# Performance work log

Measured on AMD Instinct MI355X. Metric: run time of the kernel, lower is better.

Reference implementation:

```python
import jax, jax.numpy as jnp
import numpy as np

EMBED = 1024
HEADS = 16
HEAD_DIM = EMBED // HEADS
LN_EPS = 1e-5
XNORM_GAMMA = 0.01


def xnorm(x, gamma):
    # x * gamma / ||x||_4 along last dim (keepdim)
    norm4 = jnp.sum(x ** 4, axis=-1, keepdims=True) ** 0.25
    return x * gamma / norm4


def setup_inputs() -> dict:
    key = jax.random.key(0)
    ks = jax.random.split(key, 12)
    B, S = 2, 2048
    sc_hd = 1.0 / np.sqrt(HEAD_DIM)
    sc_e = 1.0 / np.sqrt(EMBED)
    return {
        "value": jax.random.normal(ks[0], (B, S, EMBED), jnp.float32),
        "key": jax.random.normal(ks[1], (B, S, EMBED), jnp.float32),
        "query": jax.random.normal(ks[2], (B, S, EMBED), jnp.float32),
        # per-head projections, torch Linear convention: y = x @ W.T
        "Wq": jax.random.normal(ks[3], (HEAD_DIM, HEAD_DIM), jnp.float32) * sc_hd,
        "Wk": jax.random.normal(ks[4], (HEAD_DIM, HEAD_DIM), jnp.float32) * sc_hd,
        "Wv": jax.random.normal(ks[5], (HEAD_DIM, HEAD_DIM), jnp.float32) * sc_hd,
        "Wo": jax.random.normal(ks[6], (EMBED, EMBED), jnp.float32) * sc_e,
        "bo": jnp.zeros((EMBED,), jnp.float32),
        "ln_w": jnp.ones((EMBED,), jnp.float32),
        "ln_b": jnp.zeros((EMBED,), jnp.float32),
        "Wsq": jax.random.normal(ks[7], (EMBED, EMBED), jnp.float32) * sc_e,
        "bsq": jnp.zeros((EMBED,), jnp.float32),
    }


def reference(value, key, query, Wq, Wk, Wv, Wo, bo, ln_w, ln_b, Wsq, bsq):
    B, S, E = query.shape
    # split heads: [B, S, H, D]
    v = value.reshape(B, S, HEADS, HEAD_DIM)
    k = key.reshape(B, S, HEADS, HEAD_DIM)
    q = query.reshape(B, S, HEADS, HEAD_DIM)
    v = jnp.einsum('nshd,ed->nshe', v, Wv)
    k = jnp.einsum('nshd,ed->nshe', k, Wk)
    q = jnp.einsum('nshd,ed->nshe', q, Wq)
    # energy: [B, H, Sq, Sk]
    energy = jnp.einsum('nqhd,nkhd->nhqk', q, k)
    energy_n = xnorm(energy, XNORM_GAMMA)
    v_n = xnorm(v, XNORM_GAMMA)
    out = jnp.einsum('nhql,nlhd->nqhd', energy_n, v_n).reshape(B, S, E)
    attn = out @ Wo.T + bo
    # LayerNorm(attention + query) over embed dim
    x = attn + query
    mu = jnp.mean(x, axis=-1, keepdims=True)
    var = jnp.mean((x - mu) ** 2, axis=-1, keepdims=True)
    x = (x - mu) / jnp.sqrt(var + LN_EPS) * ln_w + ln_b
    # SE gating: x * sigmoid(Linear(x))
    gate = jax.nn.sigmoid(x @ Wsq.T + bsq)
    return x * gate
```

## Files before the change

kernel.cpp:

```cpp
#include <hip/hip_runtime.h>
#include <stdint.h>

#define B_ 2
#define S_ 2048
#define E_ 1024
#define H_ 16
#define HD_ 64
#define N_ (B_*S_)
#define BH_ (B_*H_)
#define GAMMA 0.01f

typedef __attribute__((ext_vector_type(8))) short bf16x8;
typedef __attribute__((ext_vector_type(4))) float f32x4;
typedef __attribute__((ext_vector_type(2))) float f32x2;
typedef __attribute__((ext_vector_type(16))) float f32x16;
typedef __attribute__((ext_vector_type(4))) unsigned int u32x4;
typedef unsigned short u16;
typedef unsigned int u32;

#define SWZ(row, kb) ((kb) ^ (((row)&7)<<4))

__device__ __forceinline__ u16 f2bf(float f){
  union { float f; u32 u; } v; v.f = f;
  return (u16)((v.u + 0x7FFFu + ((v.u>>16)&1u)) >> 16);
}

__device__ __forceinline__ float bf2f(u16 u){
  union { u32 u; float f; } v; v.u = ((u32)u)<<16; return v.f;
}

__device__ __forceinline__ u32 cvt_pk_bf16(float lo, float hi){
  u32 r; asm("v_cvt_pk_bf16_f32 %0, %1, %2" : "=v"(r) : "v"(lo), "v"(hi)); return r;
}

__device__ __forceinline__ uint4 pack8(float4 a, float4 b){
  uint4 r;
  r.x = (u32)f2bf(a.x) | ((u32)f2bf(a.y)<<16);
  r.y = (u32)f2bf(a.z) | ((u32)f2bf(a.w)<<16);
  r.z = (u32)f2bf(b.x) | ((u32)f2bf(b.y)<<16);
  r.w = (u32)f2bf(b.z) | ((u32)f2bf(b.w)<<16);
  return r;
}

__device__ __forceinline__ bf16x8 ldfrag(const unsigned char* base, int row, int kbyte){
  return *reinterpret_cast<const bf16x8*>(base + row*128 + SWZ(row, kbyte));
}

__device__ __forceinline__ void gl_lds16(const void* g, void* l){
  __builtin_amdgcn_global_load_lds(
      (const __attribute__((address_space(1))) unsigned int*)g,
      (__attribute__((address_space(3))) unsigned int*)l, 16, 0, 0);
}

__global__ __launch_bounds__(256) void k_cvt(const float* __restrict__ Wo, const float* __restrict__ Wsq,
                                             u16* __restrict__ wo16, u16* __restrict__ wsq16)
{
  int gid = blockIdx.x*256 + threadIdx.x;
  int n4 = (E_*E_)/4;
  const float4* src; ushort4* dst; int i;
  if (gid < n4){ src = (const float4*)Wo;  dst = (ushort4*)wo16;  i = gid; }
  else         { src = (const float4*)Wsq; dst = (ushort4*)wsq16; i = gid - n4; }
  float4 v = src[i];
  ushort4 p; p.x = f2bf(v.x); p.y = f2bf(v.y); p.z = f2bf(v.z); p.w = f2bf(v.w);
  dst[i] = p;
}

__device__ __forceinline__ void proj_mfma(const unsigned char* X, const unsigned char* W,
                                          int wid, int l15, int g4, f32x4 acc[4])
{
  f32x4 z = {0.f,0.f,0.f,0.f};
  acc[0]=z; acc[1]=z; acc[2]=z; acc[3]=z;
  #pragma unroll
  for (int kk=0;kk<2;++kk){
    int kbyte = kk*64 + g4*16;
    bf16x8 a = ldfrag(X, wid*16 + l15, kbyte);
    #pragma unroll
    for (int t=0;t<4;++t){
      bf16x8 w = ldfrag(W, t*16 + l15, kbyte);
      acc[t] = __builtin_amdgcn_mfma_f32_16x16x32_bf16(a, w, acc[t], 0, 0, 0);
    }
  }
}

__global__ __launch_bounds__(256) void k_proj(
    const float* __restrict__ qin, const float* __restrict__ kin, const float* __restrict__ vin,
    const float* __restrict__ Wq, const float* __restrict__ Wk, const float* __restrict__ Wv,
    u16* __restrict__ qp, u16* __restrict__ kp, u16* __restrict__ vnT)
{
  __shared__ alignas(16) unsigned char sm[57344];
  const int XQ=0, XK=8192, XV=16384, WQS=24576, WKS=32768, WVS=40960, VT=49152;
  int tid = threadIdx.x, lane = tid&63, wid = tid>>6;
  int l15 = lane&15, g4 = lane>>4;
  int tb = blockIdx.x*64;
  int h  = blockIdx.y;
  int b  = tb >> 11;
  int sbase = tb & 2047;
  int bh = b*H_ + h;

  {
    int rl = tid>>2;
    int d0 = (tid&3)*16;
    const float* xs[3] = { qin, kin, vin };
    const float* wsrc[3] = { Wq, Wk, Wv };
    const int xoff[3] = {XQ,XK,XV}, woff[3] = {WQS,WKS,WVS};
    #pragma unroll
    for (int m3=0;m3<3;++m3){
      const float4* gx = reinterpret_cast<const float4*>(xs[m3] + (size_t)(tb+rl)*E_ + h*HD_ + d0);
      float4 a=gx[0], bb=gx[1], c=gx[2], d=gx[3];
      *(uint4*)(sm + xoff[m3] + rl*128 + SWZ(rl, d0*2))    = pack8(a,bb);
      *(uint4*)(sm + xoff[m3] + rl*128 + SWZ(rl, d0*2+16)) = pack8(c,d);
      const float4* gw = reinterpret_cast<const float4*>(wsrc[m3] + rl*64 + d0);
      float4 e=gw[0], f=gw[1], g2=gw[2], h2=gw[3];
      *(uint4*)(sm + woff[m3] + rl*128 + SWZ(rl, d0*2))    = pack8(e,f);
      *(uint4*)(sm + woff[m3] + rl*128 + SWZ(rl, d0*2+16)) = pack8(g2,h2);
    }
  }
  __syncthreads();

  f32x4 acc[4];
  proj_mfma(sm+XQ, sm+WQS, wid, l15, g4, acc);
  #pragma unroll
  for (int t=0;t<4;++t)
    #pragma unroll
    for (int r=0;r<4;++r){
      int tokl = wid*16 + g4*4 + r;
      qp[((size_t)bh*S_ + sbase + tokl)*HD_ + t*16 + l15] = f2bf(acc[t][r]);
    }
  proj_mfma(sm+XK, sm+WKS, wid, l15, g4, acc);
  #pragma unroll
  for (int t=0;t<4;++t)
    #pragma unroll
    for (int r=0;r<4;++r){
      int tokl = wid*16 + g4*4 + r;
      kp[((size_t)bh*S_ + sbase + tokl)*HD_ + t*16 + l15] = f2bf(acc[t][r]);
    }
  proj_mfma(sm+XV, sm+WVS, wid, l15, g4, acc);
  {
    float p4r[4] = {0.f,0.f,0.f,0.f};
    #pragma unroll
    for (int t=0;t<4;++t)
      #pragma unroll
      for (int r=0;r<4;++r){ float e = acc[t][r]; float e2 = e*e; p4r[r] += e2*e2; }
    #pragma unroll
    for (int r=0;r<4;++r){
      float p = p4r[r];
      p += __shfl_xor(p,1); p += __shfl_xor(p,2); p += __shfl_xor(p,4); p += __shfl_xor(p,8);
      p4r[r] = GAMMA / sqrtf(sqrtf(p));
    }
    #pragma unroll
    for (int t=0;t<4;++t)
      #pragma unroll
      for (int r=0;r<4;++r){
        int tokl = wid*16 + g4*4 + r;
        int dd = t*16 + l15;
        *(u16*)(sm + VT + dd*128 + SWZ(dd, tokl*2)) = f2bf(acc[t][r] * p4r[r]);
      }
  }
  __syncthreads();
  {
    int dd = tid>>2; int c2 = tid&3;
    size_t gbase = ((size_t)bh*HD_ + dd)*S_ + sbase + c2*16;
    uint4 v0 = *(const uint4*)(sm + VT + dd*128 + SWZ(dd, c2*32));
    uint4 v1 = *(const uint4*)(sm + VT + dd*128 + SWZ(dd, c2*32+16));
    *(uint4*)(vnT + gbase)     = v0;
    *(uint4*)(vnT + gbase + 8) = v1;
  }
}

__global__ __launch_bounds__(256, 2) void k_attn(
    const u16* __restrict__ qp, const u16* __restrict__ kp,
    const u16* __restrict__ vnT, u16* __restrict__ ao)
{
  __shared__ alignas(128) unsigned char sm[49152];
  char* smc = (char*)sm;
  int tid = threadIdx.x, lane = tid&63, wv = tid>>6;
  int l31 = lane&31, hi = lane>>5;
  int qi = wv>>1, kj = wv&1;
  int L = blockIdx.x;
  int xcd = L&7, iw = L>>3;
  int bh = xcd*4 + (iw&3);
  int qx = iw>>2;
  int qb = qx*128;
  int b = bh>>4, h = bh&15;
  const u16* Kb = kp  + (size_t)bh*S_*HD_;
  const u16* Vb = vnT + (size_t)bh*HD_*S_;
  const u16* Qb = qp  + (size_t)bh*S_*HD_;
  int q0 = qb + qi*64;

  bf16x8 qf[2][4];
  #pragma unroll
  for (int f=0;f<2;++f)
    #pragma unroll
    for (int kk=0;kk<4;++kk)
      qf[f][kk] = *reinterpret_cast<const bf16x8*>(Qb + (size_t)(q0 + f*32 + l31)*HD_ + kk*16 + hi*8);

  f32x16 z16 = {};
  f32x16 o[2][2];
  #pragma unroll
  for (int f=0;f<2;++f){ o[f][0] = z16; o[f][1] = z16; }
  f32x2 p4a[2] = {{0.f,0.f},{0.f,0.f}};

  int off0 = wv*2048 + lane*16;
  int row0 = off0 >> 7, col0 = (off0 & 127) ^ ((row0 & 7) << 4);
  int off1 = off0 + 1024;
  int row1 = off1 >> 7, col1 = (off1 & 127) ^ ((row1 & 7) << 4);
  const char* kSrc0 = (const char*)Kb + row0*128 + col0;
  const char* kSrc1 = (const char*)Kb + row1*128 + col1;
  const char* vSrc0 = (const char*)Vb + (size_t)row0*4096 + col0;
  const char* vSrc1 = (const char*)Vb + (size_t)row1*4096 + col1;
  unsigned dOfs = wv*2048;

  auto STAGE = [&](int bsel, int kt){
    char* db = smc + bsel*16384 + dOfs;
    gl_lds16(kSrc0 + (size_t)kt*8192, db);
    gl_lds16(kSrc1 + (size_t)kt*8192, db + 1024);
    gl_lds16(vSrc0 + (size_t)kt*128,  db + 8192);
    gl_lds16(vSrc1 + (size_t)kt*128,  db + 8192 + 1024);
  };

  auto PACK = [&](const f32x16& e, u32 (&w)[4][2], f32x2& pa){
    #pragma unroll
    for (int j=0;j<8;++j){
      const int g=j>>1, i=j&1;
      float a = e[4*g+2*i], c = e[4*g+2*i+1];
      f32x2 pr = {a, c};
      f32x2 e2;
      asm("v_pk_mul_f32 %0, %1, %1" : "=v"(e2) : "v"(pr));
      asm("v_pk_fma_f32 %0, %1, %1, %0" : "+v"(pa) : "v"(e2));
      w[g][i] = cvt_pk_bf16(a, c);
    }
  };
  auto AFRAG = [&](u32 (&w)[4][2], int s) -> bf16x8 {
    u32 a0 = w[2*s][0], b0 = w[2*s+1][0];
    u32 a1 = w[2*s][1], b1 = w[2*s+1][1];
    asm("v_permlane32_swap_b32 %0, %1" : "+v"(a0), "+v"(b0));
    asm("v_permlane32_swap_b32 %0, %1" : "+v"(a1), "+v"(b1));
    u32x4 fw = {a0, a1, b0, b1};
    return __builtin_bit_cast(bf16x8, fw);
  };

  auto QK = [&](const unsigned char* K_, f32x16& E0, f32x16& E1){
    bf16x8 ka[4];
    #pragma unroll
    for (int kk=0;kk<4;++kk) ka[kk] = ldfrag(K_, kj*32 + l31, kk*32 + hi*16);
    E0 = z16; E1 = z16;
    __builtin_amdgcn_s_setprio(1);
    #pragma unroll
    for (int kk=0;kk<4;++kk){
      E0 = __builtin_amdgcn_mfma_f32_32x32x16_bf16(ka[kk], qf[0][kk], E0, 0,0,0);
      E1 = __builtin_amdgcn_mfma_f32_32x32x16_bf16(ka[kk], qf[1][kk], E1, 0,0,0);
    }
    __builtin_amdgcn_s_setprio(0);
  };

  auto PVF = [&](const unsigned char* V_, u32 (&w0)[4][2], u32 (&w1)[4][2]){
    bf16x8 vb[2][2];
    #pragma unroll
    for (int s=0;s<2;++s){
      vb[s][0] = ldfrag(V_, l31,    kj*64 + s*32 + hi*16);
      vb[s][1] = ldfrag(V_, 32+l31, kj*64 + s*32 + hi*16);
    }
    __builtin_amdgcn_s_setprio(1);
    #pragma unroll
    for (int s=0;s<2;++s){
      bf16x8 ef0 = AFRAG(w0, s);
      bf16x8 ef1 = AFRAG(w1, s);
      o[0][0] = __builtin_amdgcn_mfma_f32_32x32x16_bf16(ef0, vb[s][0], o[0][0], 0,0,0);
      o[0][1] = __builtin_amdgcn_mfma_f32_32x32x16_bf16(ef0, vb[s][1], o[0][1], 0,0,0);
      o[1][0] = __builtin_amdgcn_mfma_f32_32x32x16_bf16(ef1, vb[s][0], o[1][0], 0,0,0);
      o[1][1] = __builtin_amdgcn_mfma_f32_32x32x16_bf16(ef1, vb[s][1], o[1][1], 0,0,0);
    }
    __builtin_amdgcn_s_setprio(0);
  };

  const int NT = S_/64;
  STAGE(0, 0); STAGE(1, 1);
  asm volatile("s_waitcnt vmcnt(4)" ::: "memory");
  __builtin_amdgcn_s_barrier();
  asm volatile("" ::: "memory");
  STAGE(2, 2);

  f32x16 eA0, eA1, eB0, eB1;
  u32 w0[4][2], w1[4][2];
  QK(sm + 0*16384, eA0, eA1);

  #pragma unroll 1
  for (int t=0; t<NT; t+=2){
    const unsigned char* B0 = sm + (t%3)*16384;
    const unsigned char* B1 = sm + ((t+1)%3)*16384;
    PACK(eA0, w0, p4a[0]);
    PACK(eA1, w1, p4a[1]);
    PVF(B0 + 8192, w0, w1);
    if (t+1 < NT-1) { asm volatile("s_waitcnt vmcnt(4)" ::: "memory"); }
    else            { asm volatile("s_waitcnt vmcnt(0)" ::: "memory"); }
    __builtin_amdgcn_s_barrier();
    asm volatile("" ::: "memory");
    QK(B1, eB0, eB1);
    if (t+3 < NT) STAGE((t+3)%3, t+3);
    PACK(eB0, w0, p4a[0]);
    PACK(eB1, w1, p4a[1]);
    PVF(B1 + 8192, w0, w1);
    if (t+2 < NT){
      if (t+2 < NT-1) { asm volatile("s_waitcnt vmcnt(4)" ::: "memory"); }
      else            { asm volatile("s_waitcnt vmcnt(0)" ::: "memory"); }
      __builtin_amdgcn_s_barrier();
      asm volatile("" ::: "memory");
      QK(sm + ((t+2)%3)*16384, eA0, eA1);
      if (t+4 < NT) STAGE((t+4)%3, t+4);
    }
  }

  float p4f[2];
  #pragma unroll
  for (int f=0;f<2;++f) p4f[f] = p4a[f].x + p4a[f].y;

  __syncthreads();
  float* red  = (float*)smc;
  float* redp = (float*)(smc + 32768);
  if (kj==1){
    #pragma unroll
    for (int f=0;f<2;++f){
      #pragma unroll
      for (int ds=0;ds<2;++ds){
        float* dst = red + ((((qi*2+f)*2+ds)*64 + lane)*16);
        #pragma unroll
        for (int r4=0;r4<4;++r4)
          *(float4*)(dst + r4*4) = make_float4(o[f][ds][r4*4],o[f][ds][r4*4+1],o[f][ds][r4*4+2],o[f][ds][r4*4+3]);
      }
      redp[(qi*2+f)*64 + lane] = p4f[f];
    }
  }
  __syncthreads();
  if (kj==0){
    #pragma unroll
    for (int f=0;f<2;++f){
      #pragma unroll
      for (int ds=0;ds<2;++ds){
        const float* srcp = red + ((((qi*2+f)*2+ds)*64 + lane)*16);
        #pragma unroll
        for (int r4=0;r4<4;++r4){
          float4 t = *(const float4*)(srcp + r4*4);
          o[f][ds][r4*4]+=t.x; o[f][ds][r4*4+1]+=t.y; o[f][ds][r4*4+2]+=t.z; o[f][ds][r4*4+3]+=t.w;
        }
      }
      p4f[f] += redp[(qi*2+f)*64 + lane];
      p4f[f] += __shfl_xor(p4f[f], 32);
    }
    float sc0 = GAMMA * rsqrtf(sqrtf(p4f[0]));
    float sc1 = GAMMA * rsqrtf(sqrtf(p4f[1]));
    #pragma unroll
    for (int f=0;f<2;++f){
      #pragma unroll
      for (int r=0;r<16;++r){
        int qrow = (r&3) + 8*(r>>2) + 4*hi;
        float scr = __shfl(f==0 ? sc0 : sc1, qrow);
        size_t n = (size_t)b*S_ + q0 + f*32 + qrow;
        u16* dst = ao + n*E_ + h*HD_;
        dst[l31]    = f2bf(o[f][0][r] * scr);
        dst[32+l31] = f2bf(o[f][1][r] * scr);
      }
    }
  }
}

template<int MODE>
__global__ __launch_bounds__(256, 2) void k_gemm(
    const u16* __restrict__ A, const u16* __restrict__ Bw,
    const float* __restrict__ bias, const float* __restrict__ auxf,
    const u16* __restrict__ aux16, float* __restrict__ out32, u16* __restrict__ out16)
{
  __shared__ alignas(128) unsigned char sm[73728];
  char* smc = (char*)sm;
  int tid = threadIdx.x, lane = tid&63, wv = tid>>6;
  int l31 = lane&31, hi = lane>>5;
  int wr = wv>>1, wc = wv&1;
  int LL = (blockIdx.x & 7)*64 + (blockIdx.x >> 3);
  int mt = LL >> 4, nt = LL & 15;
  int m0 = mt*128, n0 = nt*64;

  int ric  = lane>>3;
  int colb = ((lane&7)*16) ^ ((ric&7)<<4);
  const char* aSrc[4]; const char* bSrc[2];
  #pragma unroll
  for (int j=0;j<4;++j)
    aSrc[j] = (const char*)A  + ((size_t)(m0 + wv*32 + 8*j + ric)*E_)*2 + colb;
  #pragma unroll
  for (int j=0;j<2;++j)
    bSrc[j] = (const char*)Bw + ((size_t)(n0 + wv*16 + 8*j + ric)*E_)*2 + colb;

  auto STAGE = [&](int bsel, int t){
    char* db = smc + bsel*24576;
    size_t kb2 = (size_t)t*128;
    #pragma unroll
    for (int j=0;j<4;++j) gl_lds16(aSrc[j] + kb2, db + (wv*4+j)*1024);
    #pragma unroll
    for (int j=0;j<2;++j) gl_lds16(bSrc[j] + kb2, db + 16384 + (wv*2+j)*1024);
  };

  f32x16 acc[2] = {{}, {}};

  const int NK = E_/64;
  STAGE(0, 0); STAGE(1, 1);

  #pragma unroll 1
  for (int t=0; t<NK; ++t){
    if (t < NK-1) { asm volatile("s_waitcnt vmcnt(6)" ::: "memory"); }
    else          { asm volatile("s_waitcnt vmcnt(0)" ::: "memory"); }
    __builtin_amdgcn_s_barrier();
    asm volatile("" ::: "memory");
    if (t+2 < NK) STAGE((t+2)%3, t+2);

    const unsigned char* Ap_ = sm + (t%3)*24576;
    const unsigned char* Bp_ = Ap_ + 16384;
    #pragma unroll
    for (int kk=0;kk<4;++kk){
      bf16x8 bfr = ldfrag(Bp_, wc*32 + l31, kk*32 + hi*16);
      bf16x8 af0 = ldfrag(Ap_, wr*64 + l31,      kk*32 + hi*16);
      bf16x8 af1 = ldfrag(Ap_, wr*64 + 32 + l31, kk*32 + hi*16);
      __builtin_amdgcn_s_setprio(1);
      acc[0] = __builtin_amdgcn_mfma_f32_32x32x16_bf16(af0, bfr, acc[0], 0,0,0);
      acc[1] = __builtin_amdgcn_mfma_f32_32x32x16_bf16(af1, bfr, acc[1], 0,0,0);
      __builtin_amdgcn_s_setprio(0);
    }
  }

  int col = n0 + wc*32 + l31;
  float bi = bias[col];
  #pragma unroll
  for (int rg=0;rg<2;++rg)
    #pragma unroll
    for (int r=0;r<16;++r){
      int mrow = m0 + wr*64 + rg*32 + (r&3) + 8*(r>>2) + 4*hi;
      size_t idx = (size_t)mrow*E_ + col;
      float v = acc[rg][r] + bi;
      if (MODE == 0){
        out16[idx] = f2bf(v + auxf[idx]);
      } else {
        float gg = 1.f/(1.f + __expf(-v));
        out32[idx] = bf2f(aux16[idx]) * gg;
      }
    }
}

__global__ __launch_bounds__(256) void k_ln(
    const u16* __restrict__ xin, const float* __restrict__ lnw, const float* __restrict__ lnb,
    u16* __restrict__ xout)
{
  __shared__ float red[8];
  __shared__ float stats[2];
  int row = blockIdx.x, tid = threadIdx.x;
  ushort4 xr = reinterpret_cast<const ushort4*>(xin + (size_t)row*E_)[tid];
  float x0 = bf2f(xr.x), x1 = bf2f(xr.y), x2 = bf2f(xr.z), x3 = bf2f(xr.w);
  float s  = x0 + x1 + x2 + x3;
  float s2 = x0*x0 + x1*x1 + x2*x2 + x3*x3;
  #pragma unroll
  for (int m=1;m<64;m<<=1){ s += __shfl_xor(s,m); s2 += __shfl_xor(s2,m); }
  if ((tid&63)==0){ red[tid>>6] = s; red[4+(tid>>6)] = s2; }
  __syncthreads();
  if (tid==0){
    float ts  = red[0]+red[1]+red[2]+red[3];
    float ts2 = red[4]+red[5]+red[6]+red[7];
    float mu  = ts * (1.f/E_);
    float var = ts2 * (1.f/E_) - mu*mu;
    stats[0] = mu; stats[1] = rsqrtf(var + 1e-5f);
  }
  __syncthreads();
  float mu = stats[0], rstd = stats[1];
  float4 w  = reinterpret_cast<const float4*>(lnw)[tid];
  float4 bb = reinterpret_cast<const float4*>(lnb)[tid];
  ushort4 p;
  p.x = f2bf((x0-mu)*rstd*w.x + bb.x);
  p.y = f2bf((x1-mu)*rstd*w.y + bb.y);
  p.z = f2bf((x2-mu)*rstd*w.z + bb.z);
  p.w = f2bf((x3-mu)*rstd*w.w + bb.w);
  reinterpret_cast<ushort4*>(xout + (size_t)row*E_)[tid] = p;
}

extern "C" void kernel_launch(void* const* d_in, const int* in_sizes, int n_in,
                              void* d_out, int out_size, void* d_ws, size_t ws_size,
                              hipStream_t stream)
{
  const float* value = (const float*)d_in[0];
  const float* key   = (const float*)d_in[1];
  const float* query = (const float*)d_in[2];
  const float* Wq    = (const float*)d_in[3];
  const float* Wk    = (const float*)d_in[4];
  const float* Wv    = (const float*)d_in[5];
  const float* Wo    = (const float*)d_in[6];
  const float* bo    = (const float*)d_in[7];
  const float* lnw   = (const float*)d_in[8];
  const float* lnb   = (const float*)d_in[9];
  const float* Wsq   = (const float*)d_in[10];
  const float* bsq   = (const float*)d_in[11];
  float* out = (float*)d_out;

  char* ws = (char*)d_ws;
  const size_t MB = 1ull<<20;
  u16*   qp     = (u16*)(ws + 0*MB);
  u16*   kp     = (u16*)(ws + 8*MB);
  u16*   vnT    = (u16*)(ws + 16*MB);
  u16*   ao     = (u16*)(ws + 24*MB);
  u16*   xres16 = (u16*)(ws + 8*MB);
  u16*   x16    = (u16*)(ws + 16*MB);
  u16*   wo16   = (u16*)(ws + 48*MB);
  u16*   wsq16  = (u16*)(ws + 50*MB);

  k_cvt <<<2048, 256, 0, stream>>>(Wo, Wsq, wo16, wsq16);
  k_proj<<<dim3(N_/64, H_), 256, 0, stream>>>(query, key, value, Wq, Wk, Wv, qp, kp, vnT);
  k_attn<<<512, 256, 0, stream>>>(qp, kp, vnT, ao);
  k_gemm<0><<<512, 256, 0, stream>>>(ao, wo16, bo, query, (const u16*)nullptr, (float*)nullptr, xres16);
  k_ln  <<<N_, 256, 0, stream>>>(xres16, lnw, lnb, x16);
  k_gemm<1><<<512, 256, 0, stream>>>(x16, wsq16, bsq, (const float*)nullptr, x16, out, (u16*)nullptr);
}
```

Before: 109.5 us.

## Fuse weight conversion into projection kernel and double-buffer 128-key attention tiles

The standalone bf16 weight-conversion kernel is folded into k_proj as 128 extra blocks, which removes one launch. The attention kernel now stages 128-key K/V tiles in a two-buffer ring (64KB LDS) instead of 64-key tiles in a three-buffer ring. It does two QK/PV sub-steps per barrier, with a new 256-byte-row swizzle for V and separate p4 accumulators. The block-to-(bh,q) mapping changes so consecutive blocks on an XCD share a head. The goal is fewer barriers and less launch overhead, at the cost of more LDS, which may limit the two-blocks-per-CU occupancy, and less prefetch depth.

```diff
diff --git a/kernel.cpp b/kernel.cpp
--- a/kernel.cpp
+++ b/kernel.cpp
@@ -45,24 +45,14 @@
 __device__ __forceinline__ bf16x8 ldfrag(const unsigned char* base, int row, int kbyte){
   return *reinterpret_cast<const bf16x8*>(base + row*128 + SWZ(row, kbyte));
 }
+__device__ __forceinline__ bf16x8 ldfragV(const unsigned char* base, int row, int col){
+  return *reinterpret_cast<const bf16x8*>(base + row*256 + (col ^ ((row&15)<<4)));
+}
 
 __device__ __forceinline__ void gl_lds16(const void* g, void* l){
   __builtin_amdgcn_global_load_lds(
       (const __attribute__((address_space(1))) unsigned int*)g,
       (__attribute__((address_space(3))) unsigned int*)l, 16, 0, 0);
-}
-
-__global__ __launch_bounds__(256) void k_cvt(const float* __restrict__ Wo, const float* __restrict__ Wsq,
-                                             u16* __restrict__ wo16, u16* __restrict__ wsq16)
-{
-  int gid = blockIdx.x*256 + threadIdx.x;
-  int n4 = (E_*E_)/4;
-  const float4* src; ushort4* dst; int i;
-  if (gid < n4){ src = (const float4*)Wo;  dst = (ushort4*)wo16;  i = gid; }
-  else         { src = (const float4*)Wsq; dst = (ushort4*)wsq16; i = gid - n4; }
-  float4 v = src[i];
-  ushort4 p; p.x = f2bf(v.x); p.y = f2bf(v.y); p.z = f2bf(v.z); p.w = f2bf(v.w);
-  dst[i] = p;
 }
 
 __device__ __forceinline__ void proj_mfma(const unsigned char* X, const unsigned char* W,
@@ -85,9 +75,24 @@
 __global__ __launch_bounds__(256) void k_proj(
     const float* __restrict__ qin, const float* __restrict__ kin, const float* __restrict__ vin,
     const float* __restrict__ Wq, const float* __restrict__ Wk, const float* __restrict__ Wv,
-    u16* __restrict__ qp, u16* __restrict__ kp, u16* __restrict__ vnT)
+    u16* __restrict__ qp, u16* __restrict__ kp, u16* __restrict__ vnT,
+    const float* __restrict__ Wo, const float* __restrict__ Wsq,
+    u16* __restrict__ wo16, u16* __restrict__ wsq16)
 {
   __shared__ alignas(16) unsigned char sm[57344];
+  if (blockIdx.y >= H_){
+    int cblk = (blockIdx.y - H_)*64 + blockIdx.x;
+    int n4 = (E_*E_)/4;
+    for (int i = cblk*256 + threadIdx.x; i < 2*n4; i += 128*256){
+      const float4* src; ushort4* dst; int j;
+      if (i < n4){ src=(const float4*)Wo;  dst=(ushort4*)wo16;  j=i; }
+      else       { src=(const float4*)Wsq; dst=(ushort4*)wsq16; j=i-n4; }
+      float4 v = src[j];
+      ushort4 p; p.x=f2bf(v.x); p.y=f2bf(v.y); p.z=f2bf(v.z); p.w=f2bf(v.w);
+      dst[j] = p;
+    }
+    return;
+  }
   const int XQ=0, XK=8192, XV=16384, WQS=24576, WKS=32768, WVS=40960, VT=49152;
   int tid = threadIdx.x, lane = tid&63, wid = tid>>6;
   int l15 = lane&15, g4 = lane>>4;
@@ -171,15 +176,15 @@
     const u16* __restrict__ qp, const u16* __restrict__ kp,
     const u16* __restrict__ vnT, u16* __restrict__ ao)
 {
-  __shared__ alignas(128) unsigned char sm[49152];
+  __shared__ alignas(128) unsigned char sm[65536];
   char* smc = (char*)sm;
   int tid = threadIdx.x, lane = tid&63, wv = tid>>6;
   int l31 = lane&31, hi = lane>>5;
   int qi = wv>>1, kj = wv&1;
   int L = blockIdx.x;
   int xcd = L&7, iw = L>>3;
-  int bh = xcd*4 + (iw&3);
-  int qx = iw>>2;
+  int bh = xcd*4 + (iw>>4);
+  int qx = iw&15;
   int qb = qx*128;
   int b = bh>>4, h = bh&15;
   const u16* Kb = kp  + (size_t)bh*S_*HD_;
@@ -199,23 +204,25 @@
   #pragma unroll
   for (int f=0;f<2;++f){ o[f][0] = z16; o[f][1] = z16; }
   f32x2 p4a[2] = {{0.f,0.f},{0.f,0.f}};
-
-  int off0 = wv*2048 + lane*16;
-  int row0 = off0 >> 7, col0 = (off0 & 127) ^ ((row0 & 7) << 4);
-  int off1 = off0 + 1024;
-  int row1 = off1 >> 7, col1 = (off1 & 127) ^ ((row1 & 7) << 4);
-  const char* kSrc0 = (const char*)Kb + row0*128 + col0;
-  const char* kSrc1 = (const char*)Kb + row1*128 + col1;
-  const char* vSrc0 = (const char*)Vb + (size_t)row0*4096 + col0;
-  const char* vSrc1 = (const char*)Vb + (size_t)row1*4096 + col1;
-  unsigned dOfs = wv*2048;
+  f32x2 p4b[2] = {{0.f,0.f},{0.f,0.f}};
+
+  const char* kSrcC[4]; const char* vSrcC[4];
+  #pragma unroll
+  for (int c=0;c<4;++c){
+    int rk = wv*32 + c*8 + (lane>>3);
+    int ck = ((lane&7)*16) ^ ((rk&7)<<4);
+    kSrcC[c] = (const char*)Kb + (size_t)rk*128 + ck;
+    int rv = wv*16 + c*4 + (lane>>4);
+    int cv = ((lane&15)*16) ^ ((rv&15)<<4);
+    vSrcC[c] = (const char*)Vb + (size_t)rv*4096 + cv;
+  }
 
   auto STAGE = [&](int bsel, int kt){
-    char* db = smc + bsel*16384 + dOfs;
-    gl_lds16(kSrc0 + (size_t)kt*8192, db);
-    gl_lds16(kSrc1 + (size_t)kt*8192, db + 1024);
-    gl_lds16(vSrc0 + (size_t)kt*128,  db + 8192);
-    gl_lds16(vSrc1 + (size_t)kt*128,  db + 8192 + 1024);
+    char* db = smc + bsel*32768 + wv*4096;
+    #pragma unroll
+    for (int c=0;c<4;++c) gl_lds16(kSrcC[c] + (size_t)kt*16384, db + c*1024);
+    #pragma unroll
+    for (int c=0;c<4;++c) gl_lds16(vSrcC[c] + (size_t)kt*256,   db + 16384 + c*1024);
   };
 
   auto PACK = [&](const f32x16& e, u32 (&w)[4][2], f32x2& pa){
@@ -239,10 +246,10 @@
     return __builtin_bit_cast(bf16x8, fw);
   };
 
-  auto QK = [&](const unsigned char* K_, f32x16& E0, f32x16& E1){
+  auto QK = [&](const unsigned char* K_, int s2, f32x16& E0, f32x16& E1){
     bf16x8 ka[4];
     #pragma unroll
-    for (int kk=0;kk<4;++kk) ka[kk] = ldfrag(K_, kj*32 + l31, kk*32 + hi*16);
+    for (int kk=0;kk<4;++kk) ka[kk] = ldfrag(K_, kj*64 + s2*32 + l31, kk*32 + hi*16);
     E0 = z16; E1 = z16;
     __builtin_amdgcn_s_setprio(1);
     #pragma unroll
@@ -253,12 +260,12 @@
     __builtin_amdgcn_s_setprio(0);
   };
 
-  auto PVF = [&](const unsigned char* V_, u32 (&w0)[4][2], u32 (&w1)[4][2]){
+  auto PVF = [&](const unsigned char* V_, int s2, u32 (&w0)[4][2], u32 (&w1)[4][2]){
     bf16x8 vb[2][2];
     #pragma unroll
     for (int s=0;s<2;++s){
-      vb[s][0] = ldfrag(V_, l31,    kj*64 + s*32 + hi*16);
-      vb[s][1] = ldfrag(V_, 32+l31, kj*64 + s*32 + hi*16);
+      vb[s][0] = ldfragV(V_, l31,    kj*128 + s2*64 + s*32 + hi*16);
+      vb[s][1] = ldfragV(V_, 32+l31, kj*128 + s2*64 + s*32 + hi*16);
     }
     __builtin_amdgcn_s_setprio(1);
     #pragma unroll
@@ -273,46 +280,39 @@
     __builtin_amdgcn_s_setprio(0);
   };
 
-  const int NT = S_/64;
+  const int NT = S_/128;
   STAGE(0, 0); STAGE(1, 1);
-  asm volatile("s_waitcnt vmcnt(4)" ::: "memory");
-  __builtin_amdgcn_s_barrier();
-  asm volatile("" ::: "memory");
-  STAGE(2, 2);
 
   f32x16 eA0, eA1, eB0, eB1;
-  u32 w0[4][2], w1[4][2];
-  QK(sm + 0*16384, eA0, eA1);
+  u32 wA0[4][2], wA1[4][2], wB0[4][2], wB1[4][2];
 
   #pragma unroll 1
-  for (int t=0; t<NT; t+=2){
-    const unsigned char* B0 = sm + (t%3)*16384;
-    const unsigned char* B1 = sm + ((t+1)%3)*16384;
-    PACK(eA0, w0, p4a[0]);
-    PACK(eA1, w1, p4a[1]);
-    PVF(B0 + 8192, w0, w1);
-    if (t+1 < NT-1) { asm volatile("s_waitcnt vmcnt(4)" ::: "memory"); }
-    else            { asm volatile("s_waitcnt vmcnt(0)" ::: "memory"); }
+  for (int t=0; t<NT; ++t){
+    if (t < NT-1) { asm volatile("s_waitcnt vmcnt(8)" ::: "memory"); }
+    else          { asm volatile("s_waitcnt vmcnt(0)" ::: "memory"); }
     __builtin_amdgcn_s_barrier();
     asm volatile("" ::: "memory");
-    QK(B1, eB0, eB1);
-    if (t+3 < NT) STAGE((t+3)%3, t+3);
-    PACK(eB0, w0, p4a[0]);
-    PACK(eB1, w1, p4a[1]);
-    PVF(B1 + 8192, w0, w1);
-    if (t+2 < NT){
-      if (t+2 < NT-1) { asm volatile("s_waitcnt vmcnt(4)" ::: "memory"); }
-      else            { asm volatile("s_waitcnt vmcnt(0)" ::: "memory"); }
-      __builtin_amdgcn_s_barrier();
-      asm volatile("" ::: "memory");
-      QK(sm + ((t+2)%3)*16384, eA0, eA1);
-      if (t+4 < NT) STAGE((t+4)%3, t+4);
-    }
+    const unsigned char* K_ = sm + (t&1)*32768;
+    const unsigned char* V_ = K_ + 16384;
+
+    QK(K_, 0, eA0, eA1);
+    QK(K_, 1, eB0, eB1);
+    PACK(eA0, wA0, p4a[0]);
+    PACK(eA1, wA1, p4a[1]);
+    PVF(V_, 0, wA0, wA1);
+    PACK(eB0, wB0, p4b[0]);
+    PACK(eB1, wB1, p4b[1]);
+    PVF(V_, 1, wB0, wB1);
+
+    asm volatile("" ::: "memory");
+    __builtin_amdgcn_s_barrier();
+    asm volatile("" ::: "memory");
+    if (t+2 < NT) STAGE(t&1, t+2);
   }
 
   float p4f[2];
   #pragma unroll
-  for (int f=0;f<2;++f) p4f[f] = p4a[f].x + p4a[f].y;
+  for (int f=0;f<2;++f) p4f[f] = p4a[f].x + p4a[f].y + p4b[f].x + p4b[f].y;
 
   __syncthreads();
   float* red  = (float*)smc;
@@ -505,8 +505,8 @@
   u16*   wo16   = (u16*)(ws + 48*MB);
   u16*   wsq16  = (u16*)(ws + 50*MB);
 
-  k_cvt <<<2048, 256, 0, stream>>>(Wo, Wsq, wo16, wsq16);
-  k_proj<<<dim3(N_/64, H_), 256, 0, stream>>>(query, key, value, Wq, Wk, Wv, qp, kp, vnT);
+  k_proj<<<dim3(N_/64, H_+2), 256, 0, stream>>>(query, key, value, Wq, Wk, Wv,
+                                                qp, kp, vnT, Wo, Wsq, wo16, wsq16);
   k_attn<<<512, 256, 0, stream>>>(qp, kp, vnT, ao);
   k_gemm<0><<<512, 256, 0, stream>>>(ao, wo16, bo, query, (const u16*)nullptr, (float*)nullptr, xres16);
   k_ln  <<<N_, 256, 0, stream>>>(xres16, lnw, lnb, x16);
```

Measured after the change: 108.6 us. No clear change (-0.8%).
